# Kernel optimization log

Measured on AMD Instinct MI355X. Metric: run time of the kernel, lower is better.

## Reference

```python
import jax, jax.numpy as jnp
import numpy as np

CH = 512      # channels
CI = CH // 4  # in_channel = 128
DILS = (1, 4, 8, 12)
GN_GROUPS = 32


def conv2d(x, w, dil=1, pad=0):
    # x: (N,Cin,H,W), w: (Cout,Cin,kh,kw)
    return jax.lax.conv_general_dilated(
        x, w, window_strides=(1, 1), padding=[(pad, pad), (pad, pad)],
        rhs_dilation=(dil, dil),
        dimension_numbers=('NCHW', 'OIHW', 'NCHW'))


def group_norm(x, gamma, beta, groups=GN_GROUPS, eps=1e-5):
    N, C, H, W = x.shape
    xg = x.reshape(N, groups, C // groups, H, W)
    mu = jnp.mean(xg, axis=(2, 3, 4), keepdims=True)
    var = jnp.var(xg, axis=(2, 3, 4), keepdims=True)
    xn = ((xg - mu) * jax.lax.rsqrt(var + eps)).reshape(N, C, H, W)
    return xn * gamma[None, :, None, None] + beta[None, :, None, None]


def dyn_branch(xd, w_cat, d):
    # dynamic filter: (N, 9, H, W), softmax over the K=9 taps per pixel
    f = jax.nn.softmax(conv2d(xd, w_cat, dil=d, pad=d), axis=1)
    N, C, H, W = xd.shape
    xp = jnp.pad(xd, ((0, 0), (0, 0), (d, d), (d, d)))
    # fused unfold + weighted sum: accumulate 9 shifted views * per-pixel weight
    out = jnp.zeros_like(xd)
    k = 0
    for i in range(3):
        for j in range(3):
            out = out + xp[:, :, i * d:i * d + H, j * d:j * d + W] * f[:, k:k + 1]
            k += 1
    return out


def setup_inputs():
    key = jax.random.key(0)
    ks = jax.random.split(key, 16)
    s = 0.05
    return {
        'x': jax.random.normal(ks[0], (4, CH, 128, 128), jnp.float32),
        'w_scale1': jax.random.normal(ks[1], (CI, CH, 1, 1), jnp.float32) * s,
        'gn1_g': jnp.ones((CI,), jnp.float32),
        'gn1_b': jnp.zeros((CI,), jnp.float32),
        'w_cata': jax.random.normal(ks[2], (9, CI, 3, 3), jnp.float32) * s,
        'w_catb': jax.random.normal(ks[3], (9, CI, 3, 3), jnp.float32) * s,
        'w_catc': jax.random.normal(ks[4], (9, CI, 3, 3), jnp.float32) * s,
        'w_catd': jax.random.normal(ks[5], (9, CI, 3, 3), jnp.float32) * s,
        'w_scale2': jax.random.normal(ks[6], (CI, 5 * CI, 1, 1), jnp.float32) * s,
        'gn2_g': jnp.ones((CI,), jnp.float32),
        'gn2_b': jnp.zeros((CI,), jnp.float32),
        'w_scale3': jax.random.normal(ks[7], (CH, CI, 1, 1), jnp.float32) * s,
        'gn3_g': jnp.ones((CH,), jnp.float32),
        'gn3_b': jnp.zeros((CH,), jnp.float32),
    }


def reference(x, w_scale1, gn1_g, gn1_b, w_cata, w_catb, w_catc, w_catd,
              w_scale2, gn2_g, gn2_b, w_scale3, gn3_g, gn3_b):
    # scale1: 1x1 conv -> GN -> ReLU
    xd = jax.nn.relu(group_norm(conv2d(x, w_scale1), gn1_g, gn1_b))
    # four dilated dynamic-filter branches (unfold + softmax-weighted reduce)
    outs = [dyn_branch(xd, w, d)
            for w, d in zip((w_cata, w_catb, w_catc, w_catd), DILS)]
    cat = jnp.concatenate([xd] + outs, axis=1)  # (N, 5*CI, H, W)
    y = jax.nn.relu(group_norm(conv2d(cat, w_scale2), gn2_g, gn2_b))
    y = jax.nn.relu(group_norm(conv2d(y, w_scale3), gn3_g, gn3_b))
    return y
```

## Files before the change

kernel.cpp:

```cpp
#include <hip/hip_runtime.h>
#include <math.h>

#define HW 16384

typedef float f32x4 __attribute__((ext_vector_type(4)));
typedef __bf16 bf16x8 __attribute__((ext_vector_type(8)));
typedef unsigned short u16x4 __attribute__((ext_vector_type(4)));
typedef unsigned short u16x8 __attribute__((ext_vector_type(8)));

__device__ __forceinline__ unsigned short f2bf(float f) {
  unsigned u = __float_as_uint(f);
  u += 0x7fffu + ((u >> 16) & 1u);
  return (unsigned short)(u >> 16);
}
__device__ __forceinline__ float bf2f(unsigned short s) {
  return __uint_as_float(((unsigned)s) << 16);
}

__global__ void prep_kernel(const float* __restrict__ w1, const float* __restrict__ w2,
                            const float* __restrict__ w3,
                            const float* __restrict__ wa, const float* __restrict__ wb,
                            const float* __restrict__ wc, const float* __restrict__ wd,
                            unsigned short* __restrict__ w1b, unsigned short* __restrict__ w2b,
                            unsigned short* __restrict__ w3b, unsigned short* __restrict__ wr) {
  int idx = blockIdx.x * 256 + threadIdx.x;
  if (idx < 65536) { w1b[idx] = f2bf(w1[idx]); }
  else if (idx < 147456) { int j = idx - 65536; w2b[j] = f2bf(w2[j]); }
  else if (idx < 212992) { int j = idx - 147456; w3b[j] = f2bf(w3[j]); }
  else if (idx < 286720) {
    int j = idx - 212992;
    int br = j / 18432, rem = j % 18432;
    int tap = rem / 2048, rem2 = rem % 2048;
    int kt = rem2 / 128, c = rem2 % 128;
    const float* w = (br == 0) ? wa : (br == 1) ? wb : (br == 2) ? wc : wd;
    float v = (kt < 9) ? w[(kt * 128 + c) * 9 + tap] : 0.f;
    wr[j] = f2bf(v);
  }
}

__device__ __forceinline__ void gn_partial_epilogue(
    f32x4 (&acc)[8], int wv, int lane, int t, int n, int blkx,
    float* __restrict__ part, float (*ps)[32], float (*pss)[32]) {
  float gs[8], gss[8];
#pragma unroll
  for (int cb = 0; cb < 8; ++cb) {
    float s = 0.f, ss = 0.f;
#pragma unroll
    for (int r = 0; r < 4; ++r) { float v = acc[cb][r]; s += v; ss += v * v; }
#pragma unroll
    for (int m = 0; m < 4; ++m) {
      const int msk[4] = {1, 2, 16, 32};
      s += __shfl_xor(s, msk[m]); ss += __shfl_xor(ss, msk[m]);
    }
    gs[cb] = s; gss[cb] = ss;
  }
  if (lane < 16 && (lane & 3) == 0) {
    int q = lane >> 2;
#pragma unroll
    for (int cb = 0; cb < 8; ++cb) { ps[wv][cb * 4 + q] = gs[cb]; pss[wv][cb * 4 + q] = gss[cb]; }
  }
  __syncthreads();
  if (t < 32) {
    float a = ps[0][t] + ps[1][t] + ps[2][t] + ps[3][t];
    float b = pss[0][t] + pss[1][t] + pss[2][t] + pss[3][t];
    float* pp = part + ((size_t)(n * 32 + t) * 256 + blkx) * 2;
    pp[0] = a; pp[1] = b;
  }
}

__global__ __launch_bounds__(256) void conv1f_kernel(
    const float* __restrict__ x, const unsigned short* __restrict__ w1b,
    unsigned short* __restrict__ outb, float* __restrict__ part) {
  __shared__ float xs[2][64][65];
  __shared__ float ps[4][32], pss[4][32];
  int t = threadIdx.x;
  int wv = t >> 6, lane = t & 63, lr = lane & 15, lg = lane >> 4;
  int n = blockIdx.y;
  int p0 = blockIdx.x * 64;
  const float* xn = x + (size_t)n * 512 * HW + p0;
  f32x4 acc[8];
#pragma unroll
  for (int cb = 0; cb < 8; ++cb) acc[cb] = (f32x4){0.f, 0.f, 0.f, 0.f};

  int ci_l = t >> 4, px4 = (t & 15) * 4;
  float4 r[4];

#pragma unroll
  for (int pass = 0; pass < 4; ++pass)
    r[pass] = *(const float4*)(xn + (size_t)(pass * 16 + ci_l) * HW + px4);
#pragma unroll
  for (int pass = 0; pass < 4; ++pass) {
    int cl = pass * 16 + ci_l;
    xs[0][cl][px4 + 0] = r[pass].x; xs[0][cl][px4 + 1] = r[pass].y;
    xs[0][cl][px4 + 2] = r[pass].z; xs[0][cl][px4 + 3] = r[pass].w;
  }

  for (int kt = 0; kt < 8; ++kt) {
    int cur = kt & 1;
    if (kt < 7) {
#pragma unroll
      for (int pass = 0; pass < 4; ++pass)
        r[pass] = *(const float4*)(xn + (size_t)((kt + 1) * 64 + pass * 16 + ci_l) * HW + px4);
    }
    __syncthreads();
#pragma unroll
    for (int ks = 0; ks < 2; ++ks) {
      bf16x8 a;
#pragma unroll
      for (int j = 0; j < 8; ++j) {
        unsigned short us = f2bf(xs[cur][ks * 32 + lg * 8 + j][wv * 16 + lr]);
        a[j] = *(__bf16*)&us;
      }
#pragma unroll
      for (int cb = 0; cb < 8; ++cb) {
        bf16x8 b = *(const bf16x8*)(w1b + (size_t)(cb * 16 + lr) * 512
                                    + kt * 64 + ks * 32 + lg * 8);
        acc[cb] = __builtin_amdgcn_mfma_f32_16x16x32_bf16(a, b, acc[cb], 0, 0, 0);
      }
    }
    if (kt < 7) {
#pragma unroll
      for (int pass = 0; pass < 4; ++pass) {
        int cl = pass * 16 + ci_l;
        xs[cur ^ 1][cl][px4 + 0] = r[pass].x; xs[cur ^ 1][cl][px4 + 1] = r[pass].y;
        xs[cur ^ 1][cl][px4 + 2] = r[pass].z; xs[cur ^ 1][cl][px4 + 3] = r[pass].w;
      }
    }
  }
  unsigned short* on = outb + (size_t)n * HW * 640;
#pragma unroll
  for (int cb = 0; cb < 8; ++cb)
#pragma unroll
    for (int r2 = 0; r2 < 4; ++r2)
      on[(size_t)(p0 + wv * 16 + lg * 4 + r2) * 640 + cb * 16 + lr] = f2bf(acc[cb][r2]);
  __syncthreads();
  gn_partial_epilogue(acc, wv, lane, t, n, blockIdx.x, part, ps, pss);
}

template<int K>
__global__ __launch_bounds__(256) void conv_pm_kernel(
    const unsigned short* __restrict__ act, const unsigned short* __restrict__ w,
    unsigned short* __restrict__ outb, float* __restrict__ part, int ldd) {
  __shared__ float ps[4][32], pss[4][32];
  int t = threadIdx.x;
  int wv = t >> 6, lane = t & 63;
  int lr = lane & 15, lg = lane >> 4;
  int n = blockIdx.y;
  int p0 = blockIdx.x * 64 + wv * 16;
  const unsigned short* an = act + (size_t)n * HW * K;
  f32x4 acc[8];
#pragma unroll
  for (int cb = 0; cb < 8; ++cb) acc[cb] = (f32x4){0.f, 0.f, 0.f, 0.f};
  const unsigned short* ap = an + (size_t)(p0 + lr) * K + lg * 8;
  const unsigned short* bp = w + (size_t)lr * K + lg * 8;
  for (int ks = 0; ks < K / 32; ++ks) {
    bf16x8 a = *(const bf16x8*)(ap + ks * 32);
#pragma unroll
    for (int cb = 0; cb < 8; ++cb) {
      bf16x8 b = *(const bf16x8*)(bp + (size_t)cb * 16 * K + ks * 32);
      acc[cb] = __builtin_amdgcn_mfma_f32_16x16x32_bf16(a, b, acc[cb], 0, 0, 0);
    }
  }
  unsigned short* on = outb + (size_t)n * HW * ldd;
#pragma unroll
  for (int cb = 0; cb < 8; ++cb)
#pragma unroll
    for (int r = 0; r < 4; ++r)
      on[(size_t)(p0 + lg * 4 + r) * ldd + cb * 16 + lr] = f2bf(acc[cb][r]);
  gn_partial_epilogue(acc, wv, lane, t, n, blockIdx.x, part, ps, pss);
}

__global__ __launch_bounds__(1024) void gnf256_kernel(
    const float* __restrict__ part, float* __restrict__ stats) {
  __shared__ float sh[1024], sh2[1024];
  int t = threadIdx.x;
  int tg = t >> 3, sub = t & 7;
  float s = 0.f, ss = 0.f;
  for (int b = sub * 32; b < sub * 32 + 32; ++b) {
    const float* pp = part + ((size_t)tg * 256 + b) * 2;
    s += pp[0]; ss += pp[1];
  }
  sh[t] = s; sh2[t] = ss;
  __syncthreads();
  if (t < 128) {
    float a = 0.f, b2 = 0.f;
#pragma unroll
    for (int i = 0; i < 8; ++i) { a += sh[t * 8 + i]; b2 += sh2[t * 8 + i]; }
    float inv = 1.f / (4.f * HW);
    float mean = a * inv, var = b2 * inv - mean * mean;
    stats[2 * t] = mean; stats[2 * t + 1] = rsqrtf(var + 1e-5f);
  }
}

__global__ __launch_bounds__(256) void gna_ip_kernel(
    unsigned short* __restrict__ dst, const float* __restrict__ stats,
    const float* __restrict__ gamma, const float* __restrict__ beta, int ldd) {
  int idx = blockIdx.x * 256 + threadIdx.x;
  int g = idx & 31;
  int p = (idx >> 5) & (HW - 1);
  int n = idx >> 19;
  unsigned short* ptr = dst + ((size_t)n * HW + p) * ldd + 4 * g;
  u16x4 v = *(u16x4*)ptr;
  int sg = n * 32 + g;
  float mean = stats[2 * sg], rstd = stats[2 * sg + 1];
  float sc0 = rstd * gamma[4 * g + 0], sc1 = rstd * gamma[4 * g + 1];
  float sc2 = rstd * gamma[4 * g + 2], sc3 = rstd * gamma[4 * g + 3];
  float sh0 = beta[4 * g + 0] - mean * sc0, sh1 = beta[4 * g + 1] - mean * sc1;
  float sh2 = beta[4 * g + 2] - mean * sc2, sh3 = beta[4 * g + 3] - mean * sc3;
  u16x4 o;
  o[0] = f2bf(fmaxf(fmaf(bf2f(v[0]), sc0, sh0), 0.f));
  o[1] = f2bf(fmaxf(fmaf(bf2f(v[1]), sc1, sh1), 0.f));
  o[2] = f2bf(fmaxf(fmaf(bf2f(v[2]), sc2, sh2), 0.f));
  o[3] = f2bf(fmaxf(fmaf(bf2f(v[3]), sc3, sh3), 0.f));
  *(u16x4*)ptr = o;
}

__global__ __launch_bounds__(256) void conv3_kernel(
    const unsigned short* __restrict__ y, const unsigned short* __restrict__ w3,
    unsigned short* __restrict__ outb, float* __restrict__ part) {
  int wv = threadIdx.x >> 6, lane = threadIdx.x & 63;
  int lr = lane & 15, lg = lane >> 4;
  int n = blockIdx.y, zc = blockIdx.z;
  int co0 = zc * 128 + wv * 32;
  int p0 = blockIdx.x * 128;
  const unsigned short* yn = y + (size_t)n * HW * 128;
  f32x4 acc[2][8];
#pragma unroll
  for (int pr = 0; pr < 2; ++pr)
#pragma unroll
    for (int cb = 0; cb < 8; ++cb) acc[pr][cb] = (f32x4){0.f, 0.f, 0.f, 0.f};
#pragma unroll
  for (int ks = 0; ks < 4; ++ks) {
    bf16x8 a0 = *(const bf16x8*)(w3 + (size_t)(co0 + lr) * 128 + ks * 32 + lg * 8);
    bf16x8 a1 = *(const bf16x8*)(w3 + (size_t)(co0 + 16 + lr) * 128 + ks * 32 + lg * 8);
#pragma unroll
    for (int cb = 0; cb < 8; ++cb) {
      bf16x8 b = *(const bf16x8*)(yn + (size_t)(p0 + cb * 16 + lr) * 128 + ks * 32 + lg * 8);
      acc[0][cb] = __builtin_amdgcn_mfma_f32_16x16x32_bf16(a0, b, acc[0][cb], 0, 0, 0);
      acc[1][cb] = __builtin_amdgcn_mfma_f32_16x16x32_bf16(a1, b, acc[1][cb], 0, 0, 0);
    }
  }
  unsigned short* on = outb + (size_t)n * 512 * HW;
  float s[2] = {0.f, 0.f}, ss[2] = {0.f, 0.f};
#pragma unroll
  for (int pr = 0; pr < 2; ++pr)
#pragma unroll
    for (int cb = 0; cb < 8; ++cb)
#pragma unroll
      for (int r = 0; r < 4; ++r) {
        float v = acc[pr][cb][r];
        on[(size_t)(co0 + pr * 16 + lg * 4 + r) * HW + p0 + cb * 16 + lr] = f2bf(v);
        s[pr] += v; ss[pr] += v * v;
      }
#pragma unroll
  for (int pr = 0; pr < 2; ++pr) {
    float a = s[pr], b = ss[pr];
    for (int m = 1; m < 64; m <<= 1) { a += __shfl_xor(a, m); b += __shfl_xor(b, m); }
    if (lane == 0) {
      float* pp = part + ((((size_t)n * 4 + zc) * 128 + blockIdx.x) * 8 + wv * 2 + pr) * 2;
      pp[0] = a; pp[1] = b;
    }
  }
}

__global__ __launch_bounds__(1024) void gnf3_kernel(
    const float* __restrict__ part, float* __restrict__ stats) {
  __shared__ float sh[1024], sh2[1024];
  int t = threadIdx.x;
  int e = t >> 3, xbs = t & 7;
  int n = e >> 5, g = e & 31;
  int zc = g >> 3, sub = g & 7;
  float s = 0.f, ss = 0.f;
  for (int xb = xbs * 16; xb < xbs * 16 + 16; ++xb) {
    const float* pp = part + ((((size_t)n * 4 + zc) * 128 + xb) * 8 + sub) * 2;
    s += pp[0]; ss += pp[1];
  }
  sh[t] = s; sh2[t] = ss;
  __syncthreads();
  if (t < 128) {
    float a = 0.f, b2 = 0.f;
#pragma unroll
    for (int i = 0; i < 8; ++i) { a += sh[t * 8 + i]; b2 += sh2[t * 8 + i]; }
    float inv = 1.f / (16.f * HW);
    float mean = a * inv, var = b2 * inv - mean * mean;
    stats[2 * t] = mean; stats[2 * t + 1] = rsqrtf(var + 1e-5f);
  }
}

__global__ __launch_bounds__(256) void gn3_apply_kernel(
    const unsigned short* __restrict__ y3b, const float* __restrict__ stats,
    const float* __restrict__ gamma, const float* __restrict__ beta,
    float* __restrict__ out) {
  size_t e8 = ((size_t)blockIdx.x * 256 + threadIdx.x) * 8;
  int n = (int)(e8 >> 23);
  int c = (int)((e8 >> 14) & 511);
  int sg = n * 32 + (c >> 4);
  float mean = stats[2 * sg], rstd = stats[2 * sg + 1];
  float scale = rstd * gamma[c];
  float shift = beta[c] - mean * scale;
  u16x8 u = *(const u16x8*)(y3b + e8);
  float4 o0, o1;
  o0.x = fmaxf(fmaf(bf2f(u[0]), scale, shift), 0.f);
  o0.y = fmaxf(fmaf(bf2f(u[1]), scale, shift), 0.f);
  o0.z = fmaxf(fmaf(bf2f(u[2]), scale, shift), 0.f);
  o0.w = fmaxf(fmaf(bf2f(u[3]), scale, shift), 0.f);
  o1.x = fmaxf(fmaf(bf2f(u[4]), scale, shift), 0.f);
  o1.y = fmaxf(fmaf(bf2f(u[5]), scale, shift), 0.f);
  o1.z = fmaxf(fmaf(bf2f(u[6]), scale, shift), 0.f);
  o1.w = fmaxf(fmaf(bf2f(u[7]), scale, shift), 0.f);
  *(float4*)(out + e8) = o0;
  *(float4*)(out + e8 + 4) = o1;
}

#define DP 136

__device__ __forceinline__ int swz16(int slot, int i) {
  return i ^ ((slot & 7) << 3);
}

__global__ __launch_bounds__(512, 4) void dynfused7_kernel(
    const unsigned short* __restrict__ cat, const unsigned short* __restrict__ wr,
    unsigned short* __restrict__ catw) {
  extern __shared__ char smem[];
  unsigned short* rowbuf = (unsigned short*)smem;
  float* fl = (float*)(smem + 3 * 88 * DP * 2);
  int t = threadIdx.x;
  int bid = blockIdx.x;
  int rh = ((bid & 7) << 5) + (bid >> 3);
  int row = rh >> 1, hw = rh & 1;
  int n = blockIdx.y >> 2, br = blockIdx.y & 3;
  int d = (br == 0) ? 1 : 4 * br;
  const unsigned short* xb = cat + (size_t)n * HW * 640;

  int rg[3] = { max(row - d, 0), row, min(row + d, 127) };
  bool rv[3] = { row - d >= 0, true, row + d < 128 };
  int cbase = hw * 64 - 12;

  {
    u16x8 vreg[9];
#pragma unroll
    for (int k = 0; k < 9; ++k) {
      int ci = t + (k << 9);
      if (k == 8 && ci >= 4224) continue;
      int s = (ci >= 2816) ? 2 : (ci >= 1408 ? 1 : 0);
      int rem = ci - s * 1408;
      int slot = rem >> 4, c = rem & 15;
      int gcol = min(max(cbase + slot, 0), 127);
      vreg[k] = *(const u16x8*)(xb + ((size_t)(rg[s] * 128 + gcol)) * 640 + c * 8);
    }
#pragma unroll
    for (int k = 0; k < 9; ++k) {
      int ci = t + (k << 9);
      if (k == 8 && ci >= 4224) continue;
      int s = (ci >= 2816) ? 2 : (ci >= 1408 ? 1 : 0);
      int rem = ci - s * 1408;
      int slot = rem >> 4, c = rem & 15;
      *(u16x8*)(rowbuf + ((size_t)s * 88 + slot) * DP + swz16(slot, c * 8)) = vreg[k];
    }
  }
  __syncthreads();

  if (t < 256) {
    int wv = t >> 6, lane = t & 63;
    int lr = lane & 15, lg = lane >> 4;
    const unsigned short* wb = wr + (size_t)br * 9 * 16 * 128;
    const bf16x8 zb = {(__bf16)0.f, (__bf16)0.f, (__bf16)0.f, (__bf16)0.f,
                       (__bf16)0.f, (__bf16)0.f, (__bf16)0.f, (__bf16)0.f};
    f32x4 acc = (f32x4){0.f, 0.f, 0.f, 0.f};
    int pxl = wv * 16 + lr;
    int gw = hw * 64 + pxl;
#pragma unroll
    for (int tap = 0; tap < 9; ++tap) {
      int s = tap / 3;
      int dw = (tap % 3 - 1) * d;
      int slot = 12 + pxl + dw;
      bool val = rv[s] && ((unsigned)(gw + dw) < 128u);
      const unsigned short* sbase = rowbuf + ((size_t)s * 88 + slot) * DP;
      const unsigned short* wt = wb + (size_t)(tap * 16 + lr) * 128 + lg * 8;
#pragma unroll
      for (int ks = 0; ks < 4; ++ks) {
        bf16x8 a = *(const bf16x8*)(sbase + swz16(slot, ks * 32 + lg * 8));
        if (!val) a = zb;
        bf16x8 b = *(const bf16x8*)(wt + ks * 32);
        acc = __builtin_amdgcn_mfma_f32_16x16x32_bf16(a, b, acc, 0, 0, 0);
      }
    }
#pragma unroll
    for (int r = 0; r < 4; ++r) {
      float v = acc[r];
      float m = (lr < 9) ? v : -3.0e38f;
#pragma unroll
      for (int msk = 1; msk < 16; msk <<= 1) m = fmaxf(m, __shfl_xor(m, msk));
      float e = (lr < 9) ? expf(v - m) : 0.f;
      float su = e;
#pragma unroll
      for (int msk = 1; msk < 16; msk <<= 1) su += __shfl_xor(su, msk);
      fl[(wv * 16 + lg * 4 + r) * 17 + lr] = e / su;
    }
  }
  __syncthreads();

  {
    int pxl = t >> 3, c8 = t & 7;
    int gw = hw * 64 + pxl;
    float oacc[16];
#pragma unroll
    for (int i = 0; i < 16; ++i) oacc[i] = 0.f;
#pragma unroll
    for (int tap = 0; tap < 9; ++tap) {
      int s = tap / 3;
      int dw = (tap % 3 - 1) * d;
      int slot = 12 + pxl + dw;
      bool val = rv[s] && ((unsigned)(gw + dw) < 128u);
      float f = val ? fl[pxl * 17 + tap] : 0.f;
      const unsigned short* sbase = rowbuf + ((size_t)s * 88 + slot) * DP;
#pragma unroll
      for (int cc = 0; cc < 2; ++cc) {
        u16x8 u = *(const u16x8*)(sbase + swz16(slot, c8 * 16 + cc * 8));
#pragma unroll
        for (int i = 0; i < 8; ++i)
          oacc[cc * 8 + i] = fmaf(f, bf2f(u[i]), oacc[cc * 8 + i]);
      }
    }
    unsigned short* orow = catw + ((size_t)n * HW + row * 128 + gw) * 640
                           + 128 * (br + 1) + c8 * 16;
#pragma unroll
    for (int cc = 0; cc < 2; ++cc) {
      u16x8 o;
#pragma unroll
      for (int i = 0; i < 8; ++i) o[i] = f2bf(oacc[cc * 8 + i]);
      *(u16x8*)(orow + cc * 8) = o;
    }
  }
}

extern "C" void kernel_launch(void* const* d_in, const int* in_sizes, int n_in,
                              void* d_out, int out_size, void* d_ws, size_t ws_size,
                              hipStream_t stream) {
  const float* x   = (const float*)d_in[0];
  const float* w1  = (const float*)d_in[1];
  const float* g1  = (const float*)d_in[2];
  const float* b1  = (const float*)d_in[3];
  const float* wca = (const float*)d_in[4];
  const float* wcb = (const float*)d_in[5];
  const float* wcc = (const float*)d_in[6];
  const float* wcd = (const float*)d_in[7];
  const float* w2  = (const float*)d_in[8];
  const float* g2  = (const float*)d_in[9];
  const float* b2  = (const float*)d_in[10];
  const float* w3  = (const float*)d_in[11];
  const float* g3  = (const float*)d_in[12];
  const float* b3  = (const float*)d_in[13];
  float* out = (float*)d_out;

  float* ws = (float*)d_ws;
  unsigned short* cat = (unsigned short*)(ws + 25165824);
  unsigned short* y2b = (unsigned short*)(ws + 8388608);
  unsigned short* y3b = (unsigned short*)(ws + 25165824);
  float* aux = ws + 46137344;
  unsigned short* w1b = (unsigned short*)(aux);
  unsigned short* w2b = (unsigned short*)(aux + 32768);
  unsigned short* w3b = (unsigned short*)(aux + 73728);
  unsigned short* wr  = (unsigned short*)(aux + 106496);
  float* part  = aux + 143360;
  float* part3 = aux + 208896;
  float* st1   = aux + 241664;
  float* st2   = aux + 241920;
  float* st3   = aux + 242176;

  dim3 blk(256);
  const int dynLds = 3 * 88 * DP * 2 + 64 * 17 * 4;
  (void)hipFuncSetAttribute((const void*)dynfused7_kernel,
                            hipFuncAttributeMaxDynamicSharedMemorySize, dynLds);

  prep_kernel<<<dim3(1120), blk, 0, stream>>>(w1, w2, w3, wca, wcb, wcc, wcd,
                                              w1b, w2b, w3b, wr);

  conv1f_kernel<<<dim3(256, 4), blk, 0, stream>>>(x, w1b, cat, part);
  gnf256_kernel<<<dim3(1), dim3(1024), 0, stream>>>(part, st1);
  gna_ip_kernel<<<dim3(8192), blk, 0, stream>>>(cat, st1, g1, b1, 640);

  dynfused7_kernel<<<dim3(256, 16), dim3(512), dynLds, stream>>>(cat, wr, cat);

  conv_pm_kernel<640><<<dim3(256, 4), blk, 0, stream>>>(cat, w2b, y2b, part, 128);
  gnf256_kernel<<<dim3(1), dim3(1024), 0, stream>>>(part, st2);
  gna_ip_kernel<<<dim3(8192), blk, 0, stream>>>(y2b, st2, g2, b2, 128);

  conv3_kernel<<<dim3(128, 4, 4), blk, 0, stream>>>(y2b, w3b, y3b, part3);
  gnf3_kernel<<<dim3(1), dim3(1024), 0, stream>>>(part3, st3);
  gn3_apply_kernel<<<dim3(16384), blk, 0, stream>>>(y3b, st3, g3, b3, out);
}
```

Before: 376.2 us.

## Shrink dynamic-filter tile to quarter rows and drop LDS swizzle

The fused dynamic-filter kernel now processes 32-pixel quarter-row tiles instead of 64-pixel half-row tiles, doubling the grid. It shrinks the LDS row buffer to 56 slots, which lets the launch bounds target 6 blocks per CU instead of 4. Thread mapping changes so each thread accumulates 8 channels for one pixel, and only two waves do the MFMA filter step. The XOR swizzle on LDS addresses is removed, relying on the 136-element row padding to limit bank conflicts. In exchange, relative halo reloading grows, since 56 slots feed 32 pixels versus 88 slots for 64.

Measured after the change: 373.2 us. No clear change (-0.8%).

```diff
diff --git a/kernel.cpp b/kernel.cpp
--- a/kernel.cpp
+++ b/kernel.cpp
@@ -313,54 +313,51 @@
 }
 
 #define DP 136
-
-__device__ __forceinline__ int swz16(int slot, int i) {
-  return i ^ ((slot & 7) << 3);
-}
-
-__global__ __launch_bounds__(512, 4) void dynfused7_kernel(
+#define DSLOTS 56
+
+__global__ __launch_bounds__(512, 6) void dynfused8_kernel(
     const unsigned short* __restrict__ cat, const unsigned short* __restrict__ wr,
     unsigned short* __restrict__ catw) {
   extern __shared__ char smem[];
   unsigned short* rowbuf = (unsigned short*)smem;
-  float* fl = (float*)(smem + 3 * 88 * DP * 2);
+  float* fl = (float*)(smem + 3 * DSLOTS * DP * 2);
   int t = threadIdx.x;
   int bid = blockIdx.x;
-  int rh = ((bid & 7) << 5) + (bid >> 3);
-  int row = rh >> 1, hw = rh & 1;
+  int rh = ((bid & 7) << 6) + (bid >> 3);
+  int row = rh >> 2, qw = rh & 3;
   int n = blockIdx.y >> 2, br = blockIdx.y & 3;
   int d = (br == 0) ? 1 : 4 * br;
   const unsigned short* xb = cat + (size_t)n * HW * 640;
 
   int rg[3] = { max(row - d, 0), row, min(row + d, 127) };
   bool rv[3] = { row - d >= 0, true, row + d < 128 };
-  int cbase = hw * 64 - 12;
+  int cbase = qw * 32 - 12;
 
   {
-    u16x8 vreg[9];
-#pragma unroll
-    for (int k = 0; k < 9; ++k) {
+    u16x8 vreg[6];
+#pragma unroll
+    for (int k = 0; k < 6; ++k) {
       int ci = t + (k << 9);
-      if (k == 8 && ci >= 4224) continue;
-      int s = (ci >= 2816) ? 2 : (ci >= 1408 ? 1 : 0);
-      int rem = ci - s * 1408;
+      if (k == 5 && ci >= 2688) continue;
+      int s = (ci >= 1792) ? 2 : (ci >= 896 ? 1 : 0);
+      int rem = ci - s * 896;
       int slot = rem >> 4, c = rem & 15;
       int gcol = min(max(cbase + slot, 0), 127);
       vreg[k] = *(const u16x8*)(xb + ((size_t)(rg[s] * 128 + gcol)) * 640 + c * 8);
     }
 #pragma unroll
-    for (int k = 0; k < 9; ++k) {
+    for (int k = 0; k < 6; ++k) {
       int ci = t + (k << 9);
-      if (k == 8 && ci >= 4224) continue;
-      int s = (ci >= 2816) ? 2 : (ci >= 1408 ? 1 : 0);
-      int rem = ci - s * 1408;
+      if (k == 5 && ci >= 2688) continue;
+      int s = (ci >= 1792) ? 2 : (ci >= 896 ? 1 : 0);
+      int rem = ci - s * 896;
       int slot = rem >> 4, c = rem & 15;
-      *(u16x8*)(rowbuf + ((size_t)s * 88 + slot) * DP + swz16(slot, c * 8)) = vreg[k];
-    }
-  }
-  __syncthreads();
-
-  if (t < 256) {
+      *(u16x8*)(rowbuf + ((size_t)s * DSLOTS + slot) * DP + c * 8) = vreg[k];
+    }
+  }
+  __syncthreads();
+
+  if (t < 128) {
     int wv = t >> 6, lane = t & 63;
     int lr = lane & 15, lg = lane >> 4;
     const unsigned short* wb = wr + (size_t)br * 9 * 16 * 128;
@@ -368,18 +365,18 @@
                        (__bf16)0.f, (__bf16)0.f, (__bf16)0.f, (__bf16)0.f};
     f32x4 acc = (f32x4){0.f, 0.f, 0.f, 0.f};
     int pxl = wv * 16 + lr;
-    int gw = hw * 64 + pxl;
+    int gw = qw * 32 + pxl;
 #pragma unroll
     for (int tap = 0; tap < 9; ++tap) {
       int s = tap / 3;
       int dw = (tap % 3 - 1) * d;
       int slot = 12 + pxl + dw;
       bool val = rv[s] && ((unsigned)(gw + dw) < 128u);
-      const unsigned short* sbase = rowbuf + ((size_t)s * 88 + slot) * DP;
+      const unsigned short* ap = rowbuf + ((size_t)s * DSLOTS + slot) * DP + lg * 8;
       const unsigned short* wt = wb + (size_t)(tap * 16 + lr) * 128 + lg * 8;
 #pragma unroll
       for (int ks = 0; ks < 4; ++ks) {
-        bf16x8 a = *(const bf16x8*)(sbase + swz16(slot, ks * 32 + lg * 8));
+        bf16x8 a = *(const bf16x8*)(ap + ks * 32);
         if (!val) a = zb;
         bf16x8 b = *(const bf16x8*)(wt + ks * 32);
         acc = __builtin_amdgcn_mfma_f32_16x16x32_bf16(a, b, acc, 0, 0, 0);
@@ -401,11 +398,11 @@
   __syncthreads();
 
   {
-    int pxl = t >> 3, c8 = t & 7;
-    int gw = hw * 64 + pxl;
-    float oacc[16];
-#pragma unroll
-    for (int i = 0; i < 16; ++i) oacc[i] = 0.f;
+    int pxl = t >> 4, c16 = t & 15;
+    int gw = qw * 32 + pxl;
+    float oacc[8];
+#pragma unroll
+    for (int i = 0; i < 8; ++i) oacc[i] = 0.f;
 #pragma unroll
     for (int tap = 0; tap < 9; ++tap) {
       int s = tap / 3;
@@ -413,24 +410,17 @@
       int slot = 12 + pxl + dw;
       bool val = rv[s] && ((unsigned)(gw + dw) < 128u);
       float f = val ? fl[pxl * 17 + tap] : 0.f;
-      const unsigned short* sbase = rowbuf + ((size_t)s * 88 + slot) * DP;
-#pragma unroll
-      for (int cc = 0; cc < 2; ++cc) {
-        u16x8 u = *(const u16x8*)(sbase + swz16(slot, c8 * 16 + cc * 8));
-#pragma unroll
-        for (int i = 0; i < 8; ++i)
-          oacc[cc * 8 + i] = fmaf(f, bf2f(u[i]), oacc[cc * 8 + i]);
-      }
+      u16x8 u = *(const u16x8*)(rowbuf + ((size_t)s * DSLOTS + slot) * DP + c16 * 8);
+#pragma unroll
+      for (int i = 0; i < 8; ++i)
+        oacc[i] = fmaf(f, bf2f(u[i]), oacc[i]);
     }
     unsigned short* orow = catw + ((size_t)n * HW + row * 128 + gw) * 640
-                           + 128 * (br + 1) + c8 * 16;
-#pragma unroll
-    for (int cc = 0; cc < 2; ++cc) {
-      u16x8 o;
-#pragma unroll
-      for (int i = 0; i < 8; ++i) o[i] = f2bf(oacc[cc * 8 + i]);
-      *(u16x8*)(orow + cc * 8) = o;
-    }
+                           + 128 * (br + 1) + c16 * 8;
+    u16x8 o;
+#pragma unroll
+    for (int i = 0; i < 8; ++i) o[i] = f2bf(oacc[i]);
+    *(u16x8*)orow = o;
   }
 }
 
@@ -469,8 +459,8 @@
   float* st3   = aux + 242176;
 
   dim3 blk(256);
-  const int dynLds = 3 * 88 * DP * 2 + 64 * 17 * 4;
-  (void)hipFuncSetAttribute((const void*)dynfused7_kernel,
+  const int dynLds = 3 * DSLOTS * DP * 2 + 32 * 17 * 4;
+  (void)hipFuncSetAttribute((const void*)dynfused8_kernel,
                             hipFuncAttributeMaxDynamicSharedMemorySize, dynLds);
 
   prep_kernel<<<dim3(1120), blk, 0, stream>>>(w1, w2, w3, wca, wcb, wcc, wcd,
@@ -480,7 +470,7 @@
   gnf256_kernel<<<dim3(1), dim3(1024), 0, stream>>>(part, st1);
   gna_ip_kernel<<<dim3(8192), blk, 0, stream>>>(cat, st1, g1, b1, 640);
 
-  dynfused7_kernel<<<dim3(256, 16), dim3(512), dynLds, stream>>>(cat, wr, cat);
+  dynfused8_kernel<<<dim3(512, 16), dim3(512), dynLds, stream>>>(cat, wr, cat);
 
   conv_pm_kernel<640><<<dim3(256, 4), blk, 0, stream>>>(cat, w2b, y2b, part, 128);
   gnf256_kernel<<<dim3(1), dim3(1024), 0, stream>>>(part, st2);
```
